# Kernel optimization log

Hardware: AMD Instinct MI355X
Metric: run time of the kernel (lower is better)

The kernel has to match this reference:

```python
import jax, jax.numpy as jnp
import numpy as np


def setup_inputs() -> dict:
    key = jax.random.key(0)
    k1, k2, k3, k4 = jax.random.split(key, 4)
    B, S, D_IN, D_OUT = 8, 2048, 4096, 4096
    inputs = jax.random.normal(k1, (B, S, D_IN), dtype=jnp.float32)
    # int8-valued weights stored as int32 (same math; original stores torch.int8)
    int8_weights = jax.random.randint(k2, (D_OUT, D_IN), -127, 128, dtype=jnp.int32)
    # realistic per-row dequant scales (small positive)
    scales = jax.random.uniform(k3, (D_OUT,), dtype=jnp.float32, minval=0.001, maxval=0.02)
    bias = jax.random.normal(k4, (1, D_OUT), dtype=jnp.float32) * 0.01
    return {"inputs": inputs, "int8_weights": int8_weights, "scales": scales, "bias": bias}


def reference(inputs, int8_weights, scales, bias):
    # converted_weights = int8_weights.to(inputs.dtype); F.linear(inputs, W) = inputs @ W.T
    w = int8_weights.astype(inputs.dtype)                      # [out, in]
    out = jnp.einsum('bsi,oi->bso', inputs, w)                 # [B, S, out]
    out = out * scales                                         # per-output-row scale
    out = out + bias                                           # bias broadcast [1, out]
    return out
```

## Files before the change

kernel.cpp:

```cpp
#include <hip/hip_runtime.h>
#include <hip/hip_bf16.h>

#define M_TOTAL 16384
#define N_TOTAL 4096
#define K_TOTAL 4096
#define NT (K_TOTAL / 128)

typedef __attribute__((ext_vector_type(4))) int i32x4;
typedef __attribute__((ext_vector_type(4))) float f32x4;

__global__ __launch_bounds__(256) void quant_a(const float* __restrict__ A,
                                               signed char* __restrict__ Aq,
                                               float* __restrict__ ascale) {
  const int row = blockIdx.x;
  const int tid = threadIdx.x;
  const float4* src = reinterpret_cast<const float4*>(A + (size_t)row * K_TOTAL) + tid * 4;
  float4 v0 = src[0], v1 = src[1], v2 = src[2], v3 = src[3];
  float m0 = fmaxf(fmaxf(fabsf(v0.x), fabsf(v0.y)), fmaxf(fabsf(v0.z), fabsf(v0.w)));
  float m1 = fmaxf(fmaxf(fabsf(v1.x), fabsf(v1.y)), fmaxf(fabsf(v1.z), fabsf(v1.w)));
  float m2 = fmaxf(fmaxf(fabsf(v2.x), fabsf(v2.y)), fmaxf(fabsf(v2.z), fabsf(v2.w)));
  float m3 = fmaxf(fmaxf(fabsf(v3.x), fabsf(v3.y)), fmaxf(fabsf(v3.z), fabsf(v3.w)));
  float amax = fmaxf(fmaxf(m0, m1), fmaxf(m2, m3));
#pragma unroll
  for (int off = 32; off > 0; off >>= 1) amax = fmaxf(amax, __shfl_xor(amax, off, 64));
  __shared__ float wmax[4];
  if ((tid & 63) == 0) wmax[tid >> 6] = amax;
  __syncthreads();
  amax = fmaxf(fmaxf(wmax[0], wmax[1]), fmaxf(wmax[2], wmax[3]));
  amax = fmaxf(amax, 1e-20f);
  const float rs = 127.0f / amax;
  if (tid == 0) ascale[row] = amax * (1.0f / 127.0f);

  int q[16];
  float a[16] = {v0.x, v0.y, v0.z, v0.w, v1.x, v1.y, v1.z, v1.w,
                 v2.x, v2.y, v2.z, v2.w, v3.x, v3.y, v3.z, v3.w};
#pragma unroll
  for (int i = 0; i < 16; ++i) {
    int t = (int)rintf(a[i] * rs);
    q[i] = t < -127 ? -127 : (t > 127 ? 127 : t);
  }
  i32x4 packed;
#pragma unroll
  for (int d = 0; d < 4; ++d)
    packed[d] = (q[d * 4] & 0xFF) | ((q[d * 4 + 1] & 0xFF) << 8) |
                ((q[d * 4 + 2] & 0xFF) << 16) | ((q[d * 4 + 3] & 0xFF) << 24);
  reinterpret_cast<i32x4*>(Aq + (size_t)row * K_TOTAL)[tid] = packed;
}

__global__ void cvt_w_i8(const int* __restrict__ W, signed char* __restrict__ Wq, int n16) {
  const int stride = gridDim.x * blockDim.x;
  for (int i = blockIdx.x * blockDim.x + threadIdx.x; i < n16; i += stride) {
    const int4* p = reinterpret_cast<const int4*>(W) + (size_t)4 * i;
    i32x4 o;
#pragma unroll
    for (int d = 0; d < 4; ++d) {
      int4 v = p[d];
      o[d] = (v.x & 0xFF) | ((v.y & 0xFF) << 8) | ((v.z & 0xFF) << 16) | ((v.w & 0xFF) << 24);
    }
    reinterpret_cast<i32x4*>(Wq)[i] = o;
  }
}

#define GLOAD_LDS16(gp, lp)                                                \
  __builtin_amdgcn_global_load_lds(                                        \
      (const __attribute__((address_space(1))) void*)(gp),                 \
      (__attribute__((address_space(3))) void*)(lp), 16, 0, 0)

#define BAR() asm volatile("s_barrier" ::: "memory")
#define VM(n) asm volatile("s_waitcnt vmcnt(" #n ")" ::: "memory")


__global__ __launch_bounds__(512, 2) void w8a16_gemm_i8(
    const signed char* __restrict__ A,
    const signed char* __restrict__ Bt,
    const float* __restrict__ ascale,
    const float* __restrict__ scales, const float* __restrict__ bias,
    float* __restrict__ C) {
  __shared__ alignas(16) unsigned char lds[131072];

  const int tid = threadIdx.x;
  const int w = tid >> 6, l = tid & 63;
  const int wr = w >> 2, wc = w & 3;
  const int bn = blockIdx.x, bm = blockIdx.y;

  const int rowq = tid >> 3;
  const int colb = ((l & 7) ^ (l >> 3)) << 4;
  const signed char* pA = A + (size_t)(bm * 256 + rowq) * K_TOTAL + colb;
  const signed char* pB = Bt + (size_t)(bn * 256 + rowq) * K_TOTAL + colb;
  unsigned char* const ldsp = lds;
  const int woff = w << 10;

#define SDA(b_, h_) (ldsp + (b_) * 65536 + (h_) * 16384 + woff)
#define SDB(b_, h_) (ldsp + (b_) * 65536 + 32768 + (h_) * 16384 + woff)
#define STAGE_A(b_, h_, t_)                                                    \
  do {                                                                         \
    GLOAD_LDS16(pA + (size_t)((h_) * 128) * K_TOTAL + (t_) * 128, SDA(b_, h_));\
    GLOAD_LDS16(pA + (size_t)((h_) * 128 + 64) * K_TOTAL + (t_) * 128,         \
                SDA(b_, h_) + 8192);                                           \
  } while (0)
#define STAGE_B(b_, h_, t_)                                                    \
  do {                                                                         \
    GLOAD_LDS16(pB + (size_t)((h_) * 128) * K_TOTAL + (t_) * 128, SDB(b_, h_));\
    GLOAD_LDS16(pB + (size_t)((h_) * 128 + 64) * K_TOTAL + (t_) * 128,         \
                SDB(b_, h_) + 8192);                                           \
  } while (0)

  const int arow = ((l & 15) << 7) + ((((l >> 4) ^ (l & 7)) & 7) << 4);

  i32x4 af[8];
  i32x4 bfr[8];
  i32x4 acc[8][4] = {{}};

#define RD_A(mh_)                                                             \
  do {                                                                        \
    const unsigned char* Ab_ = ldsp + bsel * 65536 + wr * 16384;              \
    _Pragma("unroll") for (int fm = 0; fm < 4; ++fm)                          \
        _Pragma("unroll") for (int kk = 0; kk < 2; ++kk)                      \
            af[fm * 2 + kk] = *(const i32x4*)(Ab_ + ((mh_) * 4 + fm) * 2048 + \
                                              (arow ^ (kk << 6)));            \
  } while (0)
#define RD_B(nh_)                                                             \
  do {                                                                        \
    const unsigned char* Bb_ = ldsp + bsel * 65536 + 32768 +                  \
                               (wc >> 1) * 16384 + (wc & 1) * 8192;           \
    _Pragma("unroll") for (int fn = 0; fn < 2; ++fn)                          \
        _Pragma("unroll") for (int kk = 0; kk < 2; ++kk)                      \
            bfr[((nh_) * 2 + fn) * 2 + kk] =                                  \
                *(const i32x4*)(Bb_ + ((nh_) * 2 + fn) * 2048 +               \
                                (arow ^ (kk << 6)));                          \
  } while (0)
#define QUAD(mh_, nh_)                                                        \
  do {                                                                        \
    __builtin_amdgcn_s_setprio(1);                                            \
    _Pragma("unroll") for (int m = 0; m < 4; ++m)                             \
        _Pragma("unroll") for (int n = 0; n < 2; ++n)                         \
            _Pragma("unroll") for (int kk = 0; kk < 2; ++kk)                  \
                acc[(mh_) * 4 + m][(nh_) * 2 + n] =                           \
                    __builtin_amdgcn_mfma_i32_16x16x64_i8(                    \
                        af[m * 2 + kk], bfr[((nh_) * 2 + n) * 2 + kk],        \
                        acc[(mh_) * 4 + m][(nh_) * 2 + n], 0, 0, 0);          \
    __builtin_amdgcn_s_setprio(0);                                            \
  } while (0)

  STAGE_A(0, 0, 0); STAGE_A(0, 1, 0);
  STAGE_B(0, 0, 0); STAGE_B(0, 1, 0);
  STAGE_B(1, 0, 1); STAGE_B(1, 1, 1);
  STAGE_A(1, 0, 1);
  VM(6);
  BAR();

  for (int t = 0; t < NT; ++t) {
    const int bsel = t & 1;
    RD_A(0); RD_B(0);
    if (t + 1 < NT) STAGE_A(bsel ^ 1, 1, t + 1);
    BAR();
    QUAD(0, 0);
    BAR();
    RD_B(1);
    if (t + 2 < NT) STAGE_B(bsel, 0, t + 2);
    BAR();
    QUAD(0, 1);
    BAR();
    RD_A(1);
    if (t + 2 < NT) STAGE_B(bsel, 1, t + 2);
    BAR();
    QUAD(1, 1);
    BAR();
    if (t + 2 < NT) STAGE_A(bsel, 0, t + 2);
    BAR();
    QUAD(1, 0);
    if (t < NT - 2) { VM(6); } else { VM(0); }
    BAR();
  }

  const int row0 = bm * 256 + wr * 128 + ((l >> 4) << 2);
  const int col0 = bn * 256 + wc * 64 + (l & 15);
#pragma unroll
  for (int fn = 0; fn < 4; ++fn) {
    const int col = col0 + fn * 16;
    const float sc = scales[col];
    const float bi = bias[col];
#pragma unroll
    for (int fm = 0; fm < 8; ++fm) {
      const int r = row0 + fm * 16;
      float* cp = C + (size_t)r * N_TOTAL + col;
#pragma unroll
      for (int j = 0; j < 4; ++j)
        cp[(size_t)j * N_TOTAL] = fmaf((float)acc[fm][fn][j], ascale[r + j] * sc, bi);
    }
  }
}

__global__ void naive_gemm(const float* __restrict__ A, const int* __restrict__ W,
                           const float* __restrict__ scales, const float* __restrict__ bias,
                           float* __restrict__ C) {
  size_t idx = (size_t)blockIdx.x * blockDim.x + threadIdx.x;
  if (idx >= (size_t)M_TOTAL * N_TOTAL) return;
  const int n = (int)(idx % N_TOTAL);
  const size_t m = idx / N_TOTAL;
  const float* a = A + m * (size_t)K_TOTAL;
  const int* w = W + (size_t)n * K_TOTAL;
  float s = 0.f;
  for (int k = 0; k < K_TOTAL; ++k) s = fmaf(a[k], (float)w[k], s);
  C[idx] = fmaf(s, scales[n], bias[n]);
}

extern "C" void kernel_launch(void* const* d_in, const int* in_sizes, int n_in,
                              void* d_out, int out_size, void* d_ws, size_t ws_size,
                              hipStream_t stream) {
  const float* A = (const float*)d_in[0];
  const int* W = (const int*)d_in[1];
  const float* scales = (const float*)d_in[2];
  const float* bias = (const float*)d_in[3];
  float* out = (float*)d_out;

  const size_t a_elems = (size_t)M_TOTAL * K_TOTAL;
  const size_t w_elems = (size_t)N_TOTAL * K_TOTAL;
  const size_t need = a_elems + w_elems + (size_t)M_TOTAL * sizeof(float);

  if (ws_size >= need) {
    signed char* A_q = (signed char*)d_ws;
    signed char* W_q = A_q + a_elems;
    float* a_s = (float*)(W_q + w_elems);
    quant_a<<<M_TOTAL, 256, 0, stream>>>(A, A_q, a_s);
    cvt_w_i8<<<2048, 256, 0, stream>>>(W, W_q, (int)(w_elems / 16));
    dim3 grid(N_TOTAL / 256, M_TOTAL / 256);
    w8a16_gemm_i8<<<grid, 512, 0, stream>>>(A_q, W_q, a_s, scales, bias, out);
  } else {
    size_t total = (size_t)M_TOTAL * N_TOTAL;
    naive_gemm<<<(unsigned)((total + 255) / 256), 256, 0, stream>>>(A, W, scales, bias, out);
  }
}
```

Baseline: 379.8 us.

## Coalesce quant/convert loads and remap GEMM block order across XCDs

The activation quantizer now reads float4s strided across threads (tid + 256*c) and writes packed 32-bit words, so accesses are coalesced instead of each thread reading 64 contiguous bytes. The weight converter processes one int4 per iteration and emits one packed word. The GEMM launch becomes a 1D grid whose block index is remapped so blocks dispatched round-robin to the same XCD share B/A tiles in L2. Narrower stores and more loop iterations in the converter could offset part of the gain.

```diff
diff --git a/kernel.cpp b/kernel.cpp
--- a/kernel.cpp
+++ b/kernel.cpp
@@ -9,18 +9,25 @@
 typedef __attribute__((ext_vector_type(4))) int i32x4;
 typedef __attribute__((ext_vector_type(4))) float f32x4;
 
+__device__ __forceinline__ unsigned pack4(int a, int b, int c, int d) {
+  return (a & 0xFF) | ((b & 0xFF) << 8) | ((c & 0xFF) << 16) | ((d & 0xFF) << 24);
+}
+
 __global__ __launch_bounds__(256) void quant_a(const float* __restrict__ A,
-                                               signed char* __restrict__ Aq,
+                                               unsigned* __restrict__ Aq,
                                                float* __restrict__ ascale) {
   const int row = blockIdx.x;
   const int tid = threadIdx.x;
-  const float4* src = reinterpret_cast<const float4*>(A + (size_t)row * K_TOTAL) + tid * 4;
-  float4 v0 = src[0], v1 = src[1], v2 = src[2], v3 = src[3];
-  float m0 = fmaxf(fmaxf(fabsf(v0.x), fabsf(v0.y)), fmaxf(fabsf(v0.z), fabsf(v0.w)));
-  float m1 = fmaxf(fmaxf(fabsf(v1.x), fabsf(v1.y)), fmaxf(fabsf(v1.z), fabsf(v1.w)));
-  float m2 = fmaxf(fmaxf(fabsf(v2.x), fabsf(v2.y)), fmaxf(fabsf(v2.z), fabsf(v2.w)));
-  float m3 = fmaxf(fmaxf(fabsf(v3.x), fabsf(v3.y)), fmaxf(fabsf(v3.z), fabsf(v3.w)));
-  float amax = fmaxf(fmaxf(m0, m1), fmaxf(m2, m3));
+  const float4* src = reinterpret_cast<const float4*>(A + (size_t)row * K_TOTAL);
+  float4 v[4];
+#pragma unroll
+  for (int c = 0; c < 4; ++c) v[c] = src[tid + 256 * c];
+  float amax = 0.0f;
+#pragma unroll
+  for (int c = 0; c < 4; ++c) {
+    amax = fmaxf(amax, fmaxf(fmaxf(fabsf(v[c].x), fabsf(v[c].y)),
+                             fmaxf(fabsf(v[c].z), fabsf(v[c].w))));
+  }
 #pragma unroll
   for (int off = 32; off > 0; off >>= 1) amax = fmaxf(amax, __shfl_xor(amax, off, 64));
   __shared__ float wmax[4];
@@ -31,33 +38,25 @@
   const float rs = 127.0f / amax;
   if (tid == 0) ascale[row] = amax * (1.0f / 127.0f);
 
-  int q[16];
-  float a[16] = {v0.x, v0.y, v0.z, v0.w, v1.x, v1.y, v1.z, v1.w,
-                 v2.x, v2.y, v2.z, v2.w, v3.x, v3.y, v3.z, v3.w};
-#pragma unroll
-  for (int i = 0; i < 16; ++i) {
-    int t = (int)rintf(a[i] * rs);
-    q[i] = t < -127 ? -127 : (t > 127 ? 127 : t);
-  }
-  i32x4 packed;
-#pragma unroll
-  for (int d = 0; d < 4; ++d)
-    packed[d] = (q[d * 4] & 0xFF) | ((q[d * 4 + 1] & 0xFF) << 8) |
-                ((q[d * 4 + 2] & 0xFF) << 16) | ((q[d * 4 + 3] & 0xFF) << 24);
-  reinterpret_cast<i32x4*>(Aq + (size_t)row * K_TOTAL)[tid] = packed;
-}
-
-__global__ void cvt_w_i8(const int* __restrict__ W, signed char* __restrict__ Wq, int n16) {
+  unsigned* dst = Aq + (size_t)row * (K_TOTAL / 4);
+#pragma unroll
+  for (int c = 0; c < 4; ++c) {
+    int q[4];
+    float f[4] = {v[c].x, v[c].y, v[c].z, v[c].w};
+#pragma unroll
+    for (int i = 0; i < 4; ++i) {
+      int t = (int)rintf(f[i] * rs);
+      q[i] = t < -127 ? -127 : (t > 127 ? 127 : t);
+    }
+    dst[tid + 256 * c] = pack4(q[0], q[1], q[2], q[3]);
+  }
+}
+
+__global__ void cvt_w_i8(const int* __restrict__ W, unsigned* __restrict__ Wq, int n4) {
   const int stride = gridDim.x * blockDim.x;
-  for (int i = blockIdx.x * blockDim.x + threadIdx.x; i < n16; i += stride) {
-    const int4* p = reinterpret_cast<const int4*>(W) + (size_t)4 * i;
-    i32x4 o;
-#pragma unroll
-    for (int d = 0; d < 4; ++d) {
-      int4 v = p[d];
-      o[d] = (v.x & 0xFF) | ((v.y & 0xFF) << 8) | ((v.z & 0xFF) << 16) | ((v.w & 0xFF) << 24);
-    }
-    reinterpret_cast<i32x4*>(Wq)[i] = o;
+  for (int i = blockIdx.x * blockDim.x + threadIdx.x; i < n4; i += stride) {
+    int4 v = reinterpret_cast<const int4*>(W)[i];
+    Wq[i] = pack4(v.x, v.y, v.z, v.w);
   }
 }
 
@@ -81,7 +80,10 @@
   const int tid = threadIdx.x;
   const int w = tid >> 6, l = tid & 63;
   const int wr = w >> 2, wc = w & 3;
-  const int bn = blockIdx.x, bm = blockIdx.y;
+
+  const int bid = blockIdx.x;
+  const int swz = ((bid & 7) << 7) + (bid >> 3);
+  const int bn = swz & 15, bm = swz >> 4;
 
   const int rowq = tid >> 3;
   const int colb = ((l & 7) ^ (l >> 3)) << 4;
@@ -222,10 +224,9 @@
     signed char* A_q = (signed char*)d_ws;
     signed char* W_q = A_q + a_elems;
     float* a_s = (float*)(W_q + w_elems);
-    quant_a<<<M_TOTAL, 256, 0, stream>>>(A, A_q, a_s);
-    cvt_w_i8<<<2048, 256, 0, stream>>>(W, W_q, (int)(w_elems / 16));
-    dim3 grid(N_TOTAL / 256, M_TOTAL / 256);
-    w8a16_gemm_i8<<<grid, 512, 0, stream>>>(A_q, W_q, a_s, scales, bias, out);
+    quant_a<<<M_TOTAL, 256, 0, stream>>>(A, (unsigned*)A_q, a_s);
+    cvt_w_i8<<<2048, 256, 0, stream>>>(W, (unsigned*)W_q, (int)(w_elems / 4));
+    w8a16_gemm_i8<<<1024, 512, 0, stream>>>(A_q, W_q, a_s, scales, bias, out);
   } else {
     size_t total = (size_t)M_TOTAL * N_TOTAL;
     naive_gemm<<<(unsigned)((total + 255) / 256), 256, 0, stream>>>(A, W, scales, bias, out);
```

After: 380.9 us. About the same (+0.3%).
